# Kernel tuning notes

Hardware: AMD Instinct MI355X
Metric: run time of the kernel (lower is better)

The kernel has to match this reference:

```python
import jax, jax.numpy as jnp
import numpy as np

B, T, D, H = 4096, 512, 1, 64

def _uniform(k, shape, scale):
    return jax.random.uniform(k, shape, jnp.float32, -scale, scale)

def setup_inputs() -> dict:
    key = jax.random.key(0)
    ks = jax.random.split(key, 12)
    s = 1.0 / np.sqrt(H)  # torch nn.LSTM init scale
    return {
        "x": jax.random.normal(ks[0], (B, T, D), jnp.float32),
        # layer 0 (input_size=D)
        "W_ih0": _uniform(ks[1], (4 * H, D), s),
        "W_hh0": _uniform(ks[2], (4 * H, H), s),
        "b_ih0": _uniform(ks[3], (4 * H,), s),
        "b_hh0": _uniform(ks[4], (4 * H,), s),
        # layer 1 (input_size=H)
        "W_ih1": _uniform(ks[5], (4 * H, H), s),
        "W_hh1": _uniform(ks[6], (4 * H, H), s),
        "b_ih1": _uniform(ks[7], (4 * H,), s),
        "b_hh1": _uniform(ks[8], (4 * H,), s),
        # final projection to scalar
        "W_fc": _uniform(ks[9], (1, H), s),
        "b_fc": _uniform(ks[10], (1,), s),
    }

def _lstm_layer(x_seq, W_ih, W_hh, b_ih, b_hh):
    # x_seq: (B, T, Din) -> hidden sequence (B, T, H). Gate order: i, f, g, o.
    b, t, _ = x_seq.shape
    h = W_hh.shape[1]
    # precompute input contribution for all timesteps: (T, B, 4H)
    x_proj = jnp.einsum('btd,gd->tbg', x_seq, W_ih) + b_ih + b_hh
    Whh_T = W_hh.T  # (H, 4H)

    def step(carry, xp):
        h_t, c_t = carry
        gates = xp + h_t @ Whh_T  # (B, 4H)
        i_g, f_g, g_g, o_g = jnp.split(gates, 4, axis=-1)
        i_g = jax.nn.sigmoid(i_g)
        f_g = jax.nn.sigmoid(f_g)
        g_g = jnp.tanh(g_g)
        o_g = jax.nn.sigmoid(o_g)
        c_t = f_g * c_t + i_g * g_g
        h_t = o_g * jnp.tanh(c_t)
        return (h_t, c_t), h_t

    h0 = jnp.zeros((b, h), x_seq.dtype)
    (_, _), hs = jax.lax.scan(step, (h0, h0), x_proj)  # hs: (T, B, H)
    return jnp.swapaxes(hs, 0, 1)

def reference(x, W_ih0, W_hh0, b_ih0, b_hh0, W_ih1, W_hh1, b_ih1, b_hh1, W_fc, b_fc):
    h1 = _lstm_layer(x, W_ih0, W_hh0, b_ih0, b_hh0)   # (B, T, H)
    h2 = _lstm_layer(h1, W_ih1, W_hh1, b_ih1, b_hh1)  # (B, T, H)
    last = h2[:, -1, :]                                # (B, H)
    return last @ W_fc.T + b_fc                        # (B, 1)
```

## Files before the change

### kernel.cpp

```cpp
#include <hip/hip_runtime.h>


#define TT 512
#define HH 64
#define NB 16
#define XP 516

typedef __bf16 bf16_t;
typedef bf16_t bf16x8 __attribute__((ext_vector_type(8)));
typedef float  f32x4  __attribute__((ext_vector_type(4)));
typedef float  f32x2  __attribute__((ext_vector_type(2)));

#define MFMA(A, B, C) __builtin_amdgcn_mfma_f32_16x16x32_bf16((A), (B), (C), 0, 0, 0)
#define RCPF(x) __builtin_amdgcn_rcpf(x)

#if __has_builtin(__builtin_amdgcn_exp2f)
#define EXP2F(x) __builtin_amdgcn_exp2f(x)
#else
__device__ __forceinline__ float EXP2F(float x) {
    float r;
    asm volatile("v_exp_f32 %0, %1" : "=v"(r) : "v"(x));
    return r;
}
#endif

#define SC_IFO (-1.4426950408889634f)
#define SC_G   ( 2.8853900817779268f)

__device__ __forceinline__ unsigned short f32_to_bf16_rne(float f) {
    unsigned int u = __builtin_bit_cast(unsigned int, f);
    unsigned int r = u + 0x7fffu + ((u >> 16) & 1u);
    return (unsigned short)(r >> 16);
}
__device__ __forceinline__ bf16_t bits_to_bf16(unsigned short u) {
    return __builtin_bit_cast(bf16_t, u);
}
__device__ __forceinline__ void build_frag_scaled(const float* __restrict__ p, float sc,
                                                  bf16x8& w) {
    const float4 a = *(const float4*)p;
    const float4 b = *(const float4*)(p + 4);
    float v[8] = {a.x, a.y, a.z, a.w, b.x, b.y, b.z, b.w};
#pragma unroll
    for (int jj = 0; jj < 8; ++jj)
        w[jj] = bits_to_bf16(f32_to_bf16_rne(v[jj] * sc));
}

__device__ __forceinline__ f32x2 exp2v(f32x2 v) {
    f32x2 r; r[0] = EXP2F(v[0]); r[1] = EXP2F(v[1]); return r;
}
__device__ __forceinline__ f32x2 rcpv(f32x2 v) {
    f32x2 r; r[0] = RCPF(v[0]); r[1] = RCPF(v[1]); return r;
}
__device__ __forceinline__ f32x2 cell2(const f32x4 a0, const f32x4 a1, f32x2* c) {
    f32x2 is = {a0[0], a1[0]}, fs = {a0[1], a1[1]};
    f32x2 gs = {a0[2], a1[2]}, os = {a0[3], a1[3]};
    const f32x2 pf = exp2v(fs);
    const f32x2 fg = rcpv(1.0f + pf);
    const f32x2 pi = exp2v(is);
    const f32x2 e2 = exp2v(gs);
    const f32x2 z  = (e2 - 1.0f) * rcpv((1.0f + pi) * (1.0f + e2));
    *c = fg * (*c) + z;
    const f32x2 po  = exp2v(os);
    const f32x2 e2c = exp2v((*c) * SC_G);
    return (e2c - 1.0f) * rcpv((1.0f + po) * (1.0f + e2c));
}

__device__ __forceinline__ int imin2(int a, int b) { return a < b ? a : b; }
__device__ __forceinline__ int min8of(const int* f) {
    const int4 a = *(const int4*)f;
    const int4 b = *(const int4*)(f + 4);
    return imin2(imin2(imin2(a.x, a.y), imin2(a.z, a.w)),
                 imin2(imin2(b.x, b.y), imin2(b.z, b.w)));
}

#define SPIN_BOTH(F0, F1, C0, C1)                                               \
    do {                                                                        \
        __builtin_amdgcn_s_setprio(0);                                          \
        for (;;) {                                                              \
            asm volatile("" ::: "memory");                                      \
            if ((min8of(F0) >= (C0)) & (min8of(F1) >= (C1))) break;             \
            asm volatile("" ::: "memory");                                      \
            if ((min8of(F0) >= (C0)) & (min8of(F1) >= (C1))) break;             \
            __builtin_amdgcn_s_sleep(1);                                        \
        }                                                                       \
        __builtin_amdgcn_s_setprio(1);                                          \
    } while (0)

#define SPIN_ONE(F, C)                                                          \
    do {                                                                        \
        __builtin_amdgcn_s_setprio(0);                                          \
        for (;;) {                                                              \
            asm volatile("" ::: "memory");                                      \
            if (min8of(F) >= (C)) break;                                        \
            asm volatile("" ::: "memory");                                      \
            if (min8of(F) >= (C)) break;                                        \
            __builtin_amdgcn_s_sleep(1);                                        \
        }                                                                       \
        __builtin_amdgcn_s_setprio(1);                                          \
    } while (0)

__global__ __launch_bounds__(1024, 4)
void lstm_1t_kernel(const float* __restrict__ x,
                    const float* __restrict__ Wih0, const float* __restrict__ Whh0,
                    const float* __restrict__ bih0, const float* __restrict__ bhh0,
                    const float* __restrict__ Wih1, const float* __restrict__ Whh1,
                    const float* __restrict__ bih1, const float* __restrict__ bhh1,
                    const float* __restrict__ Wfc,  const float* __restrict__ bfc,
                    float* __restrict__ out)
{
    __shared__ float xbuf[NB][XP];
    __shared__ unsigned short h0r[8][NB][64];
    __shared__ unsigned short h1r[2][NB][64];
    __shared__ float h1fin[HH][NB + 1];
    __shared__ __align__(16) int f0[8];
    __shared__ __align__(16) int f1[8];

    const int tid  = threadIdx.x;
    const int wv   = tid >> 6;
    const int lane = tid & 63;
    const int m    = lane & 15;
    const int q    = lane >> 4;
    const int m7   = m & 7;
    const int b0   = blockIdx.x * NB;
    const bool isL0 = (wv < 8);

    for (int i = tid; i < NB * TT / 4; i += 1024) {
        const int b  = i >> 7;
        const int t4 = i & 127;
        *(float4*)&xbuf[b][t4 * 4] = *(const float4*)&x[(size_t)(b0 + b) * TT + t4 * 4];
    }
    for (int i = tid; i < 8 * NB * 64; i += 1024) (&h0r[0][0][0])[i] = 0;
    for (int i = tid; i < 2 * NB * 64; i += 1024) (&h1r[0][0][0])[i] = 0;
    if (tid < 8) f0[tid] = -1;
    else if (tid < 16) f1[tid - 8] = -1;

    int roff[2];
#pragma unroll
    for (int kt = 0; kt < 2; ++kt)
        roff[kt] = m * 64 + (((4 * kt + q) ^ m7) * 8);

    const int gate_m = m & 3;
    const float scA  = (gate_m == 2) ? SC_G : SC_IFO;
    unsigned short* const H0 = &h0r[0][0][0];
    unsigned short* const H1 = &h1r[0][0][0];

    __syncthreads();

    __builtin_amdgcn_s_setprio(1);

    if (isL0) {
        const int w = wv;
        bf16x8 Ah[2][2];
        f32x4 bb0s[2], wx0s[2];
        int woff[2];
#pragma unroll
        for (int tau = 0; tau < 2; ++tau) {
            const int rowA = 64 * gate_m + 8 * w + 4 * tau + (m >> 2);
#pragma unroll
            for (int kt = 0; kt < 2; ++kt)
                build_frag_scaled(&Whh0[rowA * HH + kt * 32 + q * 8], scA, Ah[tau][kt]);
#pragma unroll
            for (int r = 0; r < 4; ++r) {
                const int row = 64 * r + 8 * w + 4 * tau + q;
                const float sc = (r == 2) ? SC_G : SC_IFO;
                bb0s[tau][r] = (bih0[row] + bhh0[row]) * sc;
                wx0s[tau][r] = Wih0[row] * sc;
            }
            const int u = 8 * w + 4 * tau + q;
            woff[tau] = m * 64 + (((u >> 3) ^ m7) * 8) + (u & 7);
        }

        f32x2 cA = {0.f, 0.f};

#pragma unroll 1
        for (int t = 0; t < TT; ++t) {
            asm volatile("" ::: "memory");
            const int c0 = t - 1;
            const int c1 = t - 8;
            const int rdy = (min8of(f0) >= c0) & (min8of(f1) >= c1);

            const float xv = xbuf[m][t];
            f32x4 a[2];
#pragma unroll
            for (int tau = 0; tau < 2; ++tau) {
#pragma unroll
                for (int r = 0; r < 4; ++r)
                    a[tau][r] = __builtin_fmaf(xv, wx0s[tau][r], bb0s[tau][r]);
            }

            if (!rdy) SPIN_BOTH(f0, f1, c0, c1);
            asm volatile("" ::: "memory");

            const int rs = ((t - 1) & 7) * (NB * 64);
            bf16x8 h0[2];
            h0[0] = *(const bf16x8*)(H0 + rs + roff[0]);
            h0[1] = *(const bf16x8*)(H0 + rs + roff[1]);

#pragma unroll
            for (int tau = 0; tau < 2; ++tau) {
                f32x4 z = {0.f, 0.f, 0.f, 0.f};
                a[tau] = MFMA(Ah[tau][0], h0[0], a[tau]);
                z      = MFMA(Ah[tau][1], h0[1], z);
                a[tau] = a[tau] + z;
            }

            const f32x2 hv = cell2(a[0], a[1], &cA);

            const int ws = (t & 7) * (NB * 64);
            H0[ws + woff[0]] = f32_to_bf16_rne(hv[0]);
            H0[ws + woff[1]] = f32_to_bf16_rne(hv[1]);

            asm volatile("s_waitcnt lgkmcnt(0)" ::: "memory");
            if (lane == 0) *(volatile int*)&f0[w] = t;
        }
    } else {
        const int uW = wv - 8;
        bf16x8 Ah[2][4];
        f32x4 bb1s[2];
        int woff[2], uu[2];
#pragma unroll
        for (int tau = 0; tau < 2; ++tau) {
            const int rowA = 64 * gate_m + 8 * uW + 4 * tau + (m >> 2);
#pragma unroll
            for (int kt = 0; kt < 2; ++kt)
                build_frag_scaled(&Wih1[rowA * HH + kt * 32 + q * 8], scA, Ah[tau][kt]);
#pragma unroll
            for (int kt = 0; kt < 2; ++kt)
                build_frag_scaled(&Whh1[rowA * HH + kt * 32 + q * 8], scA, Ah[tau][2 + kt]);
#pragma unroll
            for (int r = 0; r < 4; ++r) {
                const int row = 64 * r + 8 * uW + 4 * tau + q;
                const float sc = (r == 2) ? SC_G : SC_IFO;
                bb1s[tau][r] = (bih1[row] + bhh1[row]) * sc;
            }
            const int u = 8 * uW + 4 * tau + q;
            uu[tau]   = u;
            woff[tau] = m * 64 + (((u >> 3) ^ m7) * 8) + (u & 7);
        }

        f32x2 c1v = {0.f, 0.f};

#pragma unroll 1
        for (int t = 0; t < TT; ++t) {
            asm volatile("" ::: "memory");
            if (min8of(f0) < t) SPIN_ONE(f0, t);
            asm volatile("" ::: "memory");

            const int rs0 = (t & 7) * (NB * 64);
            bf16x8 h0[2];
            h0[0] = *(const bf16x8*)(H0 + rs0 + roff[0]);
            h0[1] = *(const bf16x8*)(H0 + rs0 + roff[1]);

            f32x4 a[2];
#pragma unroll
            for (int tau = 0; tau < 2; ++tau) {
                a[tau] = MFMA(Ah[tau][0], h0[0], bb1s[tau]);
                a[tau] = MFMA(Ah[tau][1], h0[1], a[tau]);
            }

            if (min8of(f1) < t - 1) SPIN_ONE(f1, t - 1);
            asm volatile("" ::: "memory");

            const int rs1 = ((t - 1) & 1) * (NB * 64);
            bf16x8 h1[2];
            h1[0] = *(const bf16x8*)(H1 + rs1 + roff[0]);
            h1[1] = *(const bf16x8*)(H1 + rs1 + roff[1]);

#pragma unroll
            for (int tau = 0; tau < 2; ++tau) {
                a[tau] = MFMA(Ah[tau][2], h1[0], a[tau]);
                a[tau] = MFMA(Ah[tau][3], h1[1], a[tau]);
            }

            const f32x2 hv = cell2(a[0], a[1], &c1v);
            if (t == TT - 1) {
                h1fin[uu[0]][m] = hv[0];
                h1fin[uu[1]][m] = hv[1];
            }
            const int ws = (t & 1) * (NB * 64);
            H1[ws + woff[0]] = f32_to_bf16_rne(hv[0]);
            H1[ws + woff[1]] = f32_to_bf16_rne(hv[1]);

            asm volatile("s_waitcnt lgkmcnt(0)" ::: "memory");
            if (lane == 0) *(volatile int*)&f1[uW] = t;
        }
    }

    __syncthreads();

    if (tid < NB) {
        float sacc = bfc[0];
#pragma unroll
        for (int u = 0; u < HH; ++u) sacc = fmaf(h1fin[u][tid], Wfc[u], sacc);
        out[b0 + tid] = sacc;
    }
}

extern "C" void kernel_launch(void* const* d_in, const int* in_sizes, int n_in,
                              void* d_out, int out_size, void* d_ws, size_t ws_size,
                              hipStream_t stream) {
    const float* x    = (const float*)d_in[0];
    const float* Wih0 = (const float*)d_in[1];
    const float* Whh0 = (const float*)d_in[2];
    const float* bih0 = (const float*)d_in[3];
    const float* bhh0 = (const float*)d_in[4];
    const float* Wih1 = (const float*)d_in[5];
    const float* Whh1 = (const float*)d_in[6];
    const float* bih1 = (const float*)d_in[7];
    const float* bhh1 = (const float*)d_in[8];
    const float* Wfc  = (const float*)d_in[9];
    const float* bfc  = (const float*)d_in[10];

    lstm_1t_kernel<<<dim3(4096 / NB), dim3(1024), 0, stream>>>(
        x, Wih0, Whh0, bih0, bhh0, Wih1, Whh1, bih1, bhh1, Wfc, bfc, (float*)d_out);
}
```

Measured before the change: 487.9 us.

## Replace per-wave LDS flag spinning with lockstep workgroup barriers per timestep

Removes the shared-memory progress flags and spin-wait loops between layer-0 and layer-1 waves. Both layers now run in a skewed lockstep: each iteration layer 0 computes step tt while layer 1 computes step tt-1, separated by one s_barrier per step. This drops flag polling, sleeps and priority toggling, but forces every wave to wait for the slowest one each step and removes the decoupled slack of the 8-deep ring buffer.

```diff
diff --git a/kernel.cpp b/kernel.cpp
--- a/kernel.cpp
+++ b/kernel.cpp
@@ -65,38 +65,11 @@
     return (e2c - 1.0f) * rcpv((1.0f + po) * (1.0f + e2c));
 }
 
-__device__ __forceinline__ int imin2(int a, int b) { return a < b ? a : b; }
-__device__ __forceinline__ int min8of(const int* f) {
-    const int4 a = *(const int4*)f;
-    const int4 b = *(const int4*)(f + 4);
-    return imin2(imin2(imin2(a.x, a.y), imin2(a.z, a.w)),
-                 imin2(imin2(b.x, b.y), imin2(b.z, b.w)));
-}
-
-#define SPIN_BOTH(F0, F1, C0, C1)                                               \
+#define STEP_BARRIER()                                                          \
     do {                                                                        \
-        __builtin_amdgcn_s_setprio(0);                                          \
-        for (;;) {                                                              \
-            asm volatile("" ::: "memory");                                      \
-            if ((min8of(F0) >= (C0)) & (min8of(F1) >= (C1))) break;             \
-            asm volatile("" ::: "memory");                                      \
-            if ((min8of(F0) >= (C0)) & (min8of(F1) >= (C1))) break;             \
-            __builtin_amdgcn_s_sleep(1);                                        \
-        }                                                                       \
-        __builtin_amdgcn_s_setprio(1);                                          \
-    } while (0)
-
-#define SPIN_ONE(F, C)                                                          \
-    do {                                                                        \
-        __builtin_amdgcn_s_setprio(0);                                          \
-        for (;;) {                                                              \
-            asm volatile("" ::: "memory");                                      \
-            if (min8of(F) >= (C)) break;                                        \
-            asm volatile("" ::: "memory");                                      \
-            if (min8of(F) >= (C)) break;                                        \
-            __builtin_amdgcn_s_sleep(1);                                        \
-        }                                                                       \
-        __builtin_amdgcn_s_setprio(1);                                          \
+        asm volatile("s_waitcnt lgkmcnt(0)" ::: "memory");                      \
+        __builtin_amdgcn_s_barrier();                                           \
+        asm volatile("" ::: "memory");                                          \
     } while (0)
 
 __global__ __launch_bounds__(1024, 4)
@@ -112,8 +85,6 @@
     __shared__ unsigned short h0r[8][NB][64];
     __shared__ unsigned short h1r[2][NB][64];
     __shared__ float h1fin[HH][NB + 1];
-    __shared__ __align__(16) int f0[8];
-    __shared__ __align__(16) int f1[8];
 
     const int tid  = threadIdx.x;
     const int wv   = tid >> 6;
@@ -131,8 +102,6 @@
     }
     for (int i = tid; i < 8 * NB * 64; i += 1024) (&h0r[0][0][0])[i] = 0;
     for (int i = tid; i < 2 * NB * 64; i += 1024) (&h1r[0][0][0])[i] = 0;
-    if (tid < 8) f0[tid] = -1;
-    else if (tid < 16) f1[tid - 8] = -1;
 
     int roff[2];
 #pragma unroll
@@ -145,8 +114,6 @@
     unsigned short* const H1 = &h1r[0][0][0];
 
     __syncthreads();
-
-    __builtin_amdgcn_s_setprio(1);
 
     if (isL0) {
         const int w = wv;
@@ -173,45 +140,37 @@
         f32x2 cA = {0.f, 0.f};
 
 #pragma unroll 1
-        for (int t = 0; t < TT; ++t) {
-            asm volatile("" ::: "memory");
-            const int c0 = t - 1;
-            const int c1 = t - 8;
-            const int rdy = (min8of(f0) >= c0) & (min8of(f1) >= c1);
-
-            const float xv = xbuf[m][t];
-            f32x4 a[2];
-#pragma unroll
-            for (int tau = 0; tau < 2; ++tau) {
-#pragma unroll
-                for (int r = 0; r < 4; ++r)
-                    a[tau][r] = __builtin_fmaf(xv, wx0s[tau][r], bb0s[tau][r]);
-            }
-
-            if (!rdy) SPIN_BOTH(f0, f1, c0, c1);
-            asm volatile("" ::: "memory");
-
-            const int rs = ((t - 1) & 7) * (NB * 64);
-            bf16x8 h0[2];
-            h0[0] = *(const bf16x8*)(H0 + rs + roff[0]);
-            h0[1] = *(const bf16x8*)(H0 + rs + roff[1]);
-
-#pragma unroll
-            for (int tau = 0; tau < 2; ++tau) {
-                f32x4 z = {0.f, 0.f, 0.f, 0.f};
-                a[tau] = MFMA(Ah[tau][0], h0[0], a[tau]);
-                z      = MFMA(Ah[tau][1], h0[1], z);
-                a[tau] = a[tau] + z;
-            }
-
-            const f32x2 hv = cell2(a[0], a[1], &cA);
-
-            const int ws = (t & 7) * (NB * 64);
-            H0[ws + woff[0]] = f32_to_bf16_rne(hv[0]);
-            H0[ws + woff[1]] = f32_to_bf16_rne(hv[1]);
-
-            asm volatile("s_waitcnt lgkmcnt(0)" ::: "memory");
-            if (lane == 0) *(volatile int*)&f0[w] = t;
+        for (int tt = 0; tt <= TT; ++tt) {
+            if (tt < TT) {
+                const int rs = ((tt - 1) & 7) * (NB * 64);
+                bf16x8 h0[2];
+                h0[0] = *(const bf16x8*)(H0 + rs + roff[0]);
+                h0[1] = *(const bf16x8*)(H0 + rs + roff[1]);
+
+                const float xv = xbuf[m][tt];
+                f32x4 a[2];
+#pragma unroll
+                for (int tau = 0; tau < 2; ++tau) {
+#pragma unroll
+                    for (int r = 0; r < 4; ++r)
+                        a[tau][r] = __builtin_fmaf(xv, wx0s[tau][r], bb0s[tau][r]);
+                }
+
+#pragma unroll
+                for (int tau = 0; tau < 2; ++tau) {
+                    f32x4 z = {0.f, 0.f, 0.f, 0.f};
+                    a[tau] = MFMA(Ah[tau][0], h0[0], a[tau]);
+                    z      = MFMA(Ah[tau][1], h0[1], z);
+                    a[tau] = a[tau] + z;
+                }
+
+                const f32x2 hv = cell2(a[0], a[1], &cA);
+
+                const int ws = (tt & 7) * (NB * 64);
+                H0[ws + woff[0]] = f32_to_bf16_rne(hv[0]);
+                H0[ws + woff[1]] = f32_to_bf16_rne(hv[1]);
+            }
+            STEP_BARRIER();
         }
     } else {
         const int uW = wv - 8;
@@ -241,48 +200,36 @@
         f32x2 c1v = {0.f, 0.f};
 
 #pragma unroll 1
-        for (int t = 0; t < TT; ++t) {
-            asm volatile("" ::: "memory");
-            if (min8of(f0) < t) SPIN_ONE(f0, t);
-            asm volatile("" ::: "memory");
-
-            const int rs0 = (t & 7) * (NB * 64);
-            bf16x8 h0[2];
-            h0[0] = *(const bf16x8*)(H0 + rs0 + roff[0]);
-            h0[1] = *(const bf16x8*)(H0 + rs0 + roff[1]);
-
-            f32x4 a[2];
-#pragma unroll
-            for (int tau = 0; tau < 2; ++tau) {
-                a[tau] = MFMA(Ah[tau][0], h0[0], bb1s[tau]);
-                a[tau] = MFMA(Ah[tau][1], h0[1], a[tau]);
-            }
-
-            if (min8of(f1) < t - 1) SPIN_ONE(f1, t - 1);
-            asm volatile("" ::: "memory");
-
-            const int rs1 = ((t - 1) & 1) * (NB * 64);
-            bf16x8 h1[2];
-            h1[0] = *(const bf16x8*)(H1 + rs1 + roff[0]);
-            h1[1] = *(const bf16x8*)(H1 + rs1 + roff[1]);
-
-#pragma unroll
-            for (int tau = 0; tau < 2; ++tau) {
-                a[tau] = MFMA(Ah[tau][2], h1[0], a[tau]);
-                a[tau] = MFMA(Ah[tau][3], h1[1], a[tau]);
-            }
-
-            const f32x2 hv = cell2(a[0], a[1], &c1v);
-            if (t == TT - 1) {
-                h1fin[uu[0]][m] = hv[0];
-                h1fin[uu[1]][m] = hv[1];
-            }
-            const int ws = (t & 1) * (NB * 64);
-            H1[ws + woff[0]] = f32_to_bf16_rne(hv[0]);
-            H1[ws + woff[1]] = f32_to_bf16_rne(hv[1]);
-
-            asm volatile("s_waitcnt lgkmcnt(0)" ::: "memory");
-            if (lane == 0) *(volatile int*)&f1[uW] = t;
+        for (int tt = 0; tt <= TT; ++tt) {
+            if (tt >= 1) {
+                const int tm = tt - 1;
+                const int rs0 = (tm & 7) * (NB * 64);
+                const int rs1 = ((tm - 1) & 1) * (NB * 64);
+                bf16x8 h0[2], h1[2];
+                h0[0] = *(const bf16x8*)(H0 + rs0 + roff[0]);
+                h0[1] = *(const bf16x8*)(H0 + rs0 + roff[1]);
+                h1[0] = *(const bf16x8*)(H1 + rs1 + roff[0]);
+                h1[1] = *(const bf16x8*)(H1 + rs1 + roff[1]);
+
+                f32x4 a[2];
+#pragma unroll
+                for (int tau = 0; tau < 2; ++tau) {
+                    a[tau] = MFMA(Ah[tau][0], h0[0], bb1s[tau]);
+                    a[tau] = MFMA(Ah[tau][1], h0[1], a[tau]);
+                    a[tau] = MFMA(Ah[tau][2], h1[0], a[tau]);
+                    a[tau] = MFMA(Ah[tau][3], h1[1], a[tau]);
+                }
+
+                const f32x2 hv = cell2(a[0], a[1], &c1v);
+                if (tm == TT - 1) {
+                    h1fin[uu[0]][m] = hv[0];
+                    h1fin[uu[1]][m] = hv[1];
+                }
+                const int ws = (tm & 1) * (NB * 64);
+                H1[ws + woff[0]] = f32_to_bf16_rne(hv[0]);
+                H1[ws + woff[1]] = f32_to_bf16_rne(hv[1]);
+            }
+            STEP_BARRIER();
         }
     }
 
```

Result: faster. 420.1 us (-13.9%).
